# Performance work log

Hardware: AMD Instinct MI355X
Metric: run time of the kernel (lower is better)

Reference implementation:

```python
import jax, jax.numpy as jnp
import numpy as np

EPS = 1e-8
D = 1024      # embedding_dim
NH = 4        # num_heads
HD = D // NH  # head_dim
B, S = 4, 2048


def setup_inputs() -> dict:
    key = jax.random.key(0)
    k1, k2 = jax.random.split(key)
    x = jax.random.normal(k1, (B, S, 4 * D), dtype=jnp.float32)
    # small-init std = sqrt(2/(5*head_dim)) as in reset_parameters
    std = float(np.sqrt(2.0 / (5.0 * HD)))
    gate_weights = jax.random.normal(k2, (4, NH, HD, HD), dtype=jnp.float32) * std
    # biases: z,i,o zero; f gets powerlaw init (block 0 of 1 -> exponent 0.3)
    term = jnp.arange(HD, dtype=jnp.float32) / (HD - 1.0)
    f_bias = -(-5.0 + 12.0 * term ** 0.3)  # [HD]
    gate_biases = jnp.zeros((4, NH, HD), dtype=jnp.float32)
    gate_biases = gate_biases.at[2].set(jnp.broadcast_to(f_bias, (NH, HD)))
    return {"x_gate_inputs": x, "gate_weights": gate_weights, "gate_biases": gate_biases}


def _slstm_forward(x, W, biases):
    Bn, Sn, _ = x.shape
    # split into 4 gate pre-activations and apply headwise linear per gate
    xg = x.reshape(Bn, Sn, 4, NH, HD)           # gate order z,i,f,o along axis 2
    xg = jnp.moveaxis(xg, 2, 0)                  # [4,B,S,NH,HD]
    # headwise projection: einsum over head-in dim, per gate g and head h
    gates = jnp.einsum('gbshi,ghoi->gbsho', xg, W) + biases[:, None, None]  # [4,B,S,NH,HD]
    gates = jnp.moveaxis(gates, 2, 0)            # [S,4,B,NH,HD] for scan over time

    h0 = jnp.zeros((Bn, NH, HD), dtype=x.dtype)
    carry0 = (h0, h0, h0, jnp.zeros((Bn, NH, HD), dtype=jnp.float32))

    def step(carry, g_t):
        h, c, n, m = carry
        z_b, i_b, f_b, o_b = g_t[0], g_t[1], g_t[2], g_t[3]
        z_val = jnp.tanh(z_b)
        o_val = jax.nn.sigmoid(o_b)
        # faithful to original: exp then log(.+EPS), in m-state dtype (fp32)
        log_f = jnp.log(jnp.exp(f_b).astype(jnp.float32) + EPS)
        log_i = jnp.log(jnp.exp(i_b).astype(jnp.float32) + EPS)
        m_new = jnp.maximum(log_f + m, log_i)
        i_hat = jnp.exp(log_i - m_new).astype(x.dtype)
        f_hat = jnp.exp(log_f + m - m_new).astype(x.dtype)
        c_new = f_hat * c + i_hat * z_val
        n_new = f_hat * n + i_hat
        h_new = o_val * (c_new / (n_new + EPS))
        return (h_new, c_new, n_new, m_new), h_new

    (h_f, c_f, n_f, m_f), hs = jax.lax.scan(step, carry0, gates)
    h_seq = jnp.moveaxis(hs, 0, 1)               # [B,S,NH,HD]
    return h_seq, (h_f, c_f, n_f, m_f)


def reference(x_gate_inputs, gate_weights, gate_biases):
    h_seq, (h_f, c_f, n_f, m_f) = _slstm_forward(x_gate_inputs, gate_weights, gate_biases)
    return h_seq, h_f, c_f, n_f, m_f
```

## Files before the change

### kernel.cpp

```cpp
#include <hip/hip_runtime.h>
#include <cstdint>

#define S_LEN   2048
#define BATCH   4
#define NCH     4096
#define PLANE   ((size_t)S_LEN * NCH)
#define CHUNK   32
#define NCHUNK  64
#define SN      ((size_t)NCHUNK * NCH)
#define EPS     1e-8f

using bf16x8 = __attribute__((ext_vector_type(8))) short;
using f32x4  = __attribute__((ext_vector_type(4))) float;
typedef unsigned short u16;

__device__ __forceinline__ short f2bf(float f) {
  uint32_t u = __builtin_bit_cast(uint32_t, f);
  u += 0x7fffu + ((u >> 16) & 1u);
  return (short)(u >> 16);
}
__device__ __forceinline__ float bf2f(u16 u) {
  return __builtin_bit_cast(float, (uint32_t)u << 16);
}

__global__ __launch_bounds__(1024) void gates_gemm3(
    const float* __restrict__ x, const float* __restrict__ W,
    const float* __restrict__ bias,
    u16* __restrict__ gz16, float* __restrict__ gi, float* __restrict__ gf,
    u16* __restrict__ go16) {
  __shared__ u16 As[2][16 * 264];

  const int gh  = blockIdx.x;
  const int rg  = blockIdx.y;
  const int g   = gh >> 2, hh = gh & 3;
  const int tid = threadIdx.x;
  const int wave = tid >> 6, lane = tid & 63;
  const int l16 = lane & 15, quad = lane >> 4;
  const int n0  = wave * 16;
  const int row0 = rg * 256;

  bf16x8 Bf[8];
  {
    const float* wp = W + ((size_t)gh << 16) + (n0 + l16) * 256 + quad * 8;
#pragma unroll
    for (int kt = 0; kt < 8; ++kt) {
      float4 w0 = *(const float4*)(wp + kt * 32);
      float4 w1 = *(const float4*)(wp + kt * 32 + 4);
      bf16x8 b;
      b[0] = f2bf(w0.x); b[1] = f2bf(w0.y); b[2] = f2bf(w0.z); b[3] = f2bf(w0.w);
      b[4] = f2bf(w1.x); b[5] = f2bf(w1.y); b[6] = f2bf(w1.z); b[7] = f2bf(w1.w);
      Bf[kt] = b;
    }
  }
  const float bv = bias[gh * 256 + n0 + l16];

  const int sr = tid >> 6, sc = tid & 63;
  const float* sbase = x + (size_t)(row0 + sr) * 4096 + g * 1024 + hh * 256 + sc * 4;

  float4 sreg;
  auto gload = [&](int t) { sreg = *(const float4*)(sbase + (size_t)t * 16 * 4096); };
  auto swrite = [&](int buf) {
    ushort4 u;
    u.x = (u16)f2bf(sreg.x); u.y = (u16)f2bf(sreg.y);
    u.z = (u16)f2bf(sreg.z); u.w = (u16)f2bf(sreg.w);
    *(ushort4*)&As[buf][sr * 264 + sc * 4] = u;
  };

  gload(0); swrite(0);
  __syncthreads();

  for (int t = 0; t < 16; ++t) {
    if (t + 1 < 16) gload(t + 1);

    f32x4 acc = (f32x4){0.f, 0.f, 0.f, 0.f};
#pragma unroll
    for (int kt = 0; kt < 8; ++kt) {
      bf16x8 a = *(const bf16x8*)&As[t & 1][l16 * 264 + kt * 32 + quad * 8];
      acc = __builtin_amdgcn_mfma_f32_16x16x32_bf16(a, Bf[kt], acc, 0, 0, 0);
    }

#pragma unroll
    for (int rr = 0; rr < 4; ++rr) {
      int rowi = row0 + t * 16 + quad * 4 + rr;
      int sx = rowi & (S_LEN - 1);
      int bx = rowi >> 11;
      size_t idx = (size_t)sx * NCH + bx * 1024 + hh * 256 + n0 + l16;
      float v = acc[rr] + bv;
      if (g == 1)      gi[idx] = v;
      else if (g == 2) gf[idx] = v;
      else if (g == 0) {
        float tz = 1.f - 2.f * __builtin_amdgcn_rcpf(1.f + __expf(2.f * v));
        gz16[idx] = (u16)f2bf(tz);
      } else {
        float s = __builtin_amdgcn_rcpf(1.f + __expf(-v));
        go16[idx] = (u16)f2bf(s);
      }
    }

    if (t + 1 < 16) {
      swrite((t + 1) & 1);
      __syncthreads();
    }
  }
}

__global__ __launch_bounds__(256) void scan_pass1(
    const u16* __restrict__ gz16, const float* __restrict__ gi,
    const float* __restrict__ gf, float* __restrict__ sums) {
  const int t  = blockIdx.x * 256 + threadIdx.x;
  const int ch = t & (NCH - 1);
  const int ck = t >> 12;
  const size_t base = (size_t)ck * CHUNK * NCH + ch;

  float A = 0.f, Bv = -1e30f, D = 0.f, Dn = 0.f;

  float z0[8], i0[8], f0[8], z1[8], i1[8], f1[8];
#pragma unroll
  for (int j = 0; j < 8; ++j) {
    size_t off = base + (size_t)j * NCH;
    z0[j] = bf2f(gz16[off]); i0[j] = gi[off]; f0[j] = gf[off];
  }

  auto step = [&](float z, float i, float f) {
    float Bn = fmaxf(Bv + f, i);
    float e1 = __expf(Bv + f - Bn);
    float e2 = __expf(i - Bn);
    D  = e1 * D + e2 * z;
    Dn = e1 * Dn + e2;
    A += f;
    Bv = Bn;
  };

  for (int gb = 0; gb < 4; gb += 2) {
#pragma unroll
    for (int j = 0; j < 8; ++j) {
      size_t off = base + (size_t)((gb + 1) * 8 + j) * NCH;
      z1[j] = bf2f(gz16[off]); i1[j] = gi[off]; f1[j] = gf[off];
    }
#pragma unroll
    for (int j = 0; j < 8; ++j) step(z0[j], i0[j], f0[j]);
    if (gb + 2 < 4) {
#pragma unroll
      for (int j = 0; j < 8; ++j) {
        size_t off = base + (size_t)((gb + 2) * 8 + j) * NCH;
        z0[j] = bf2f(gz16[off]); i0[j] = gi[off]; f0[j] = gf[off];
      }
    }
#pragma unroll
    for (int j = 0; j < 8; ++j) step(z1[j], i1[j], f1[j]);
  }

  const size_t idx = (size_t)ck * NCH + ch;
  sums[idx]          = A;
  sums[SN + idx]     = Bv;
  sums[2 * SN + idx] = D;
  sums[3 * SN + idx] = Dn;
}

__global__ __launch_bounds__(256) void scan_pass2(
    const float* __restrict__ sums, float* __restrict__ ent) {
  const int ch = blockIdx.x * 256 + threadIdx.x;
  float c = 0.f, n = 0.f, m = 0.f;

  float A0 = sums[ch], B0 = sums[SN + ch], D0 = sums[2 * SN + ch], N0 = sums[3 * SN + ch];
  for (int k = 0; k < NCHUNK; ++k) {
    float A1 = 0.f, B1 = 0.f, D1 = 0.f, N1 = 0.f;
    if (k + 1 < NCHUNK) {
      size_t ni = (size_t)(k + 1) * NCH + ch;
      A1 = sums[ni]; B1 = sums[SN + ni]; D1 = sums[2 * SN + ni]; N1 = sums[3 * SN + ni];
    }
    size_t idx = (size_t)k * NCH + ch;
    ent[idx]          = c;
    ent[SN + idx]     = n;
    ent[2 * SN + idx] = m;
    float mo = fmaxf(m + A0, B0);
    float ea = __expf(m + A0 - mo);
    float eb = __expf(B0 - mo);
    c = ea * c + eb * D0;
    n = ea * n + eb * N0;
    m = mo;
    A0 = A1; B0 = B1; D0 = D1; N0 = N1;
  }
}

__global__ __launch_bounds__(256) void scan_pass3(
    const u16* __restrict__ gz16, const float* __restrict__ gi,
    const float* __restrict__ gf, const u16* __restrict__ go16,
    const float* __restrict__ ent, float* __restrict__ out) {
  const int t  = blockIdx.x * 256 + threadIdx.x;
  const int ch = t & (NCH - 1);
  const int ck = t >> 12;

  const size_t idx0 = (size_t)ck * NCH + ch;
  float c = ent[idx0];
  float n = ent[SN + idx0];
  float m = ent[2 * SN + idx0];

  const int b = ch >> 10, d = ch & 1023;
  const size_t base = (size_t)ck * CHUNK * NCH + ch;
  float* hout = out + (size_t)b * (S_LEN * 1024) + (size_t)(ck * CHUNK) * 1024 + d;

  float hv = 0.f;
  float z0[8], i0[8], f0[8], o0[8], z1[8], i1[8], f1[8], o1[8];
#pragma unroll
  for (int j = 0; j < 8; ++j) {
    size_t off = base + (size_t)j * NCH;
    z0[j] = bf2f(gz16[off]); i0[j] = gi[off]; f0[j] = gf[off]; o0[j] = bf2f(go16[off]);
  }

  auto step = [&](float z, float i, float f, float o, int s) {
    float mn = fmaxf(f + m, i);
    float fh = __expf(f + m - mn);
    float ih = __expf(i - mn);
    c = fh * c + ih * z;
    n = fh * n + ih;
    m = mn;
    hv = o * c * __builtin_amdgcn_rcpf(n + EPS);
    hout[(size_t)s * 1024] = hv;
  };

  for (int gb = 0; gb < 4; gb += 2) {
#pragma unroll
    for (int j = 0; j < 8; ++j) {
      size_t off = base + (size_t)((gb + 1) * 8 + j) * NCH;
      z1[j] = bf2f(gz16[off]); i1[j] = gi[off]; f1[j] = gf[off]; o1[j] = bf2f(go16[off]);
    }
#pragma unroll
    for (int j = 0; j < 8; ++j) step(z0[j], i0[j], f0[j], o0[j], gb * 8 + j);
    if (gb + 2 < 4) {
#pragma unroll
      for (int j = 0; j < 8; ++j) {
        size_t off = base + (size_t)((gb + 2) * 8 + j) * NCH;
        z0[j] = bf2f(gz16[off]); i0[j] = gi[off]; f0[j] = gf[off]; o0[j] = bf2f(go16[off]);
      }
    }
#pragma unroll
    for (int j = 0; j < 8; ++j) step(z1[j], i1[j], f1[j], o1[j], (gb + 1) * 8 + j);
  }

  if (ck == NCHUNK - 1) {
    float* fin = out + (size_t)BATCH * S_LEN * 1024;
    fin[ch]            = hv;
    fin[NCH + ch]      = c;
    fin[2 * NCH + ch]  = n;
    fin[3 * NCH + ch]  = m;
  }
}

extern "C" void kernel_launch(void* const* d_in, const int* in_sizes, int n_in,
                              void* d_out, int out_size, void* d_ws, size_t ws_size,
                              hipStream_t stream) {
  const float* x    = (const float*)d_in[0];
  const float* W    = (const float*)d_in[1];
  const float* bias = (const float*)d_in[2];
  float* out = (float*)d_out;

  u16*   gz16 = (u16*)d_ws;
  float* gi   = (float*)(gz16 + PLANE);
  float* gf   = gi + PLANE;
  u16*   go16 = (u16*)(gf + PLANE);
  float* sums = (float*)(go16 + PLANE);
  float* ent  = sums + 4 * SN;

  gates_gemm3<<<dim3(16, 32), dim3(1024), 0, stream>>>(x, W, bias, gz16, gi, gf, go16);
  scan_pass1<<<dim3(1024), dim3(256), 0, stream>>>(gz16, gi, gf, sums);
  scan_pass2<<<dim3(16), dim3(256), 0, stream>>>(sums, ent);
  scan_pass3<<<dim3(1024), dim3(256), 0, stream>>>(gz16, gi, gf, go16, ent, out);
}
```

Measured before the change: 277.8 us.

## Parallelize chunk-carry scan across wave lanes and double GEMM row tile

The pass-2 chunk combine changes from a per-channel sequential loop over 64 chunks into a warp-level Hillis-Steele prefix scan using shuffles, one lane per chunk. This removes a long serial dependency chain that ran on only 16 blocks. The gate GEMM also processes 32 rows per iteration with two MFMA accumulators, a padded LDS stride and deeper register prefetch, so fewer barriers are needed. The cost is more shuffle/exp work per channel and higher register use in the GEMM.

After: 308.3 us. +11.0%, slower.

```diff
diff --git a/kernel.cpp b/kernel.cpp
--- a/kernel.cpp
+++ b/kernel.cpp
@@ -9,6 +9,7 @@
 #define NCHUNK  64
 #define SN      ((size_t)NCHUNK * NCH)
 #define EPS     1e-8f
+#define LDST    280
 
 using bf16x8 = __attribute__((ext_vector_type(8))) short;
 using f32x4  = __attribute__((ext_vector_type(4))) float;
@@ -23,12 +24,12 @@
   return __builtin_bit_cast(float, (uint32_t)u << 16);
 }
 
-__global__ __launch_bounds__(1024) void gates_gemm3(
+__global__ __launch_bounds__(1024) void gates_gemm4(
     const float* __restrict__ x, const float* __restrict__ W,
     const float* __restrict__ bias,
     u16* __restrict__ gz16, float* __restrict__ gi, float* __restrict__ gf,
     u16* __restrict__ go16) {
-  __shared__ u16 As[2][16 * 264];
+  __shared__ u16 As[2][32 * LDST];
 
   const int gh  = blockIdx.x;
   const int rg  = blockIdx.y;
@@ -57,50 +58,63 @@
   const int sr = tid >> 6, sc = tid & 63;
   const float* sbase = x + (size_t)(row0 + sr) * 4096 + g * 1024 + hh * 256 + sc * 4;
 
-  float4 sreg;
-  auto gload = [&](int t) { sreg = *(const float4*)(sbase + (size_t)t * 16 * 4096); };
-  auto swrite = [&](int buf) {
-    ushort4 u;
-    u.x = (u16)f2bf(sreg.x); u.y = (u16)f2bf(sreg.y);
-    u.z = (u16)f2bf(sreg.z); u.w = (u16)f2bf(sreg.w);
-    *(ushort4*)&As[buf][sr * 264 + sc * 4] = u;
+  float4 pre[2][2];
+  auto gload = [&](int slot, int t) {
+    const float* p = sbase + (size_t)t * 32 * 4096;
+    pre[slot][0] = *(const float4*)p;
+    pre[slot][1] = *(const float4*)(p + 16 * 4096);
   };
-
-  gload(0); swrite(0);
+  auto swrite = [&](int slot, int buf) {
+#pragma unroll
+    for (int rh = 0; rh < 2; ++rh) {
+      float4 v = pre[slot][rh];
+      ushort4 u;
+      u.x = (u16)f2bf(v.x); u.y = (u16)f2bf(v.y);
+      u.z = (u16)f2bf(v.z); u.w = (u16)f2bf(v.w);
+      *(ushort4*)&As[buf][(sr + rh * 16) * LDST + sc * 4] = u;
+    }
+  };
+
+  gload(0, 0);
+  gload(1, 1);
+  swrite(0, 0);
   __syncthreads();
 
-  for (int t = 0; t < 16; ++t) {
-    if (t + 1 < 16) gload(t + 1);
-
-    f32x4 acc = (f32x4){0.f, 0.f, 0.f, 0.f};
+  for (int t = 0; t < 8; ++t) {
+    if (t + 2 < 8) gload(t & 1, t + 2);
+    if (t + 1 < 8) swrite((t + 1) & 1, (t + 1) & 1);
+
+    f32x4 acc0 = (f32x4){0.f, 0.f, 0.f, 0.f};
+    f32x4 acc1 = (f32x4){0.f, 0.f, 0.f, 0.f};
 #pragma unroll
     for (int kt = 0; kt < 8; ++kt) {
-      bf16x8 a = *(const bf16x8*)&As[t & 1][l16 * 264 + kt * 32 + quad * 8];
-      acc = __builtin_amdgcn_mfma_f32_16x16x32_bf16(a, Bf[kt], acc, 0, 0, 0);
-    }
-
-#pragma unroll
-    for (int rr = 0; rr < 4; ++rr) {
-      int rowi = row0 + t * 16 + quad * 4 + rr;
-      int sx = rowi & (S_LEN - 1);
-      int bx = rowi >> 11;
-      size_t idx = (size_t)sx * NCH + bx * 1024 + hh * 256 + n0 + l16;
-      float v = acc[rr] + bv;
-      if (g == 1)      gi[idx] = v;
-      else if (g == 2) gf[idx] = v;
-      else if (g == 0) {
-        float tz = 1.f - 2.f * __builtin_amdgcn_rcpf(1.f + __expf(2.f * v));
-        gz16[idx] = (u16)f2bf(tz);
-      } else {
-        float s = __builtin_amdgcn_rcpf(1.f + __expf(-v));
-        go16[idx] = (u16)f2bf(s);
+      bf16x8 a0 = *(const bf16x8*)&As[t & 1][l16 * LDST + kt * 32 + quad * 8];
+      bf16x8 a1 = *(const bf16x8*)&As[t & 1][(l16 + 16) * LDST + kt * 32 + quad * 8];
+      acc0 = __builtin_amdgcn_mfma_f32_16x16x32_bf16(a0, Bf[kt], acc0, 0, 0, 0);
+      acc1 = __builtin_amdgcn_mfma_f32_16x16x32_bf16(a1, Bf[kt], acc1, 0, 0, 0);
+    }
+
+#pragma unroll
+    for (int rt = 0; rt < 2; ++rt) {
+#pragma unroll
+      for (int rr = 0; rr < 4; ++rr) {
+        int rowi = row0 + t * 32 + rt * 16 + quad * 4 + rr;
+        int sx = rowi & (S_LEN - 1);
+        int bx = rowi >> 11;
+        size_t idx = (size_t)sx * NCH + bx * 1024 + hh * 256 + n0 + l16;
+        float v = (rt ? acc1[rr] : acc0[rr]) + bv;
+        if (g == 1)      gi[idx] = v;
+        else if (g == 2) gf[idx] = v;
+        else if (g == 0) {
+          float tz = 1.f - 2.f * __builtin_amdgcn_rcpf(1.f + __expf(2.f * v));
+          gz16[idx] = (u16)f2bf(tz);
+        } else {
+          float s = __builtin_amdgcn_rcpf(1.f + __expf(-v));
+          go16[idx] = (u16)f2bf(s);
+        }
       }
     }
-
-    if (t + 1 < 16) {
-      swrite((t + 1) & 1);
-      __syncthreads();
-    }
+    __syncthreads();
   }
 }
 
@@ -159,28 +173,51 @@
 
 __global__ __launch_bounds__(256) void scan_pass2(
     const float* __restrict__ sums, float* __restrict__ ent) {
-  const int ch = blockIdx.x * 256 + threadIdx.x;
-  float c = 0.f, n = 0.f, m = 0.f;
-
-  float A0 = sums[ch], B0 = sums[SN + ch], D0 = sums[2 * SN + ch], N0 = sums[3 * SN + ch];
-  for (int k = 0; k < NCHUNK; ++k) {
-    float A1 = 0.f, B1 = 0.f, D1 = 0.f, N1 = 0.f;
-    if (k + 1 < NCHUNK) {
-      size_t ni = (size_t)(k + 1) * NCH + ch;
-      A1 = sums[ni]; B1 = sums[SN + ni]; D1 = sums[2 * SN + ni]; N1 = sums[3 * SN + ni];
-    }
-    size_t idx = (size_t)k * NCH + ch;
-    ent[idx]          = c;
-    ent[SN + idx]     = n;
-    ent[2 * SN + idx] = m;
-    float mo = fmaxf(m + A0, B0);
-    float ea = __expf(m + A0 - mo);
-    float eb = __expf(B0 - mo);
-    c = ea * c + eb * D0;
-    n = ea * n + eb * N0;
-    m = mo;
-    A0 = A1; B0 = B1; D0 = D1; N0 = N1;
-  }
+  const int gt   = blockIdx.x * 256 + threadIdx.x;
+  const int ch   = gt >> 6;
+  const int lane = gt & 63;
+
+  const size_t idx = (size_t)lane * NCH + ch;
+  float A = sums[idx];
+  float B = sums[SN + idx];
+  float D = sums[2 * SN + idx];
+  float N = sums[3 * SN + idx];
+
+#pragma unroll
+  for (int d = 1; d < 64; d <<= 1) {
+    float A1 = __shfl_up(A, d, 64);
+    float B1 = __shfl_up(B, d, 64);
+    float D1 = __shfl_up(D, d, 64);
+    float N1 = __shfl_up(N, d, 64);
+    if (lane >= d) {
+      float Bn = fmaxf(B1 + A, B);
+      float e1 = __expf(B1 + A - Bn);
+      float e2 = __expf(B - Bn);
+      D = e1 * D1 + e2 * D;
+      N = e1 * N1 + e2 * N;
+      A = A + A1;
+      B = Bn;
+    }
+  }
+
+  float Ae = __shfl_up(A, 1, 64);
+  float Be = __shfl_up(B, 1, 64);
+  float De = __shfl_up(D, 1, 64);
+  float Ne = __shfl_up(N, 1, 64);
+
+  float c, n, m;
+  if (lane == 0) {
+    c = 0.f; n = 0.f; m = 0.f;
+  } else {
+    m = fmaxf(Ae, Be);
+    float eb = __expf(Be - m);
+    c = eb * De;
+    n = eb * Ne;
+  }
+
+  ent[idx]          = c;
+  ent[SN + idx]     = n;
+  ent[2 * SN + idx] = m;
 }
 
 __global__ __launch_bounds__(256) void scan_pass3(
@@ -262,8 +299,8 @@
   float* sums = (float*)(go16 + PLANE);
   float* ent  = sums + 4 * SN;
 
-  gates_gemm3<<<dim3(16, 32), dim3(1024), 0, stream>>>(x, W, bias, gz16, gi, gf, go16);
+  gates_gemm4<<<dim3(16, 32), dim3(1024), 0, stream>>>(x, W, bias, gz16, gi, gf, go16);
   scan_pass1<<<dim3(1024), dim3(256), 0, stream>>>(gz16, gi, gf, sums);
-  scan_pass2<<<dim3(16), dim3(256), 0, stream>>>(sums, ent);
+  scan_pass2<<<dim3(1024), dim3(256), 0, stream>>>(sums, ent);
   scan_pass3<<<dim3(1024), dim3(256), 0, stream>>>(gz16, gi, gf, go16, ent, out);
 }
```

## Store i/f gates as fp16, halve scan chunk, parallelize chunk-carry scan via shuffles

Applied to the files above, without the earlier changes.

Stores the i and f gate pre-activations as fp16 instead of fp32, cutting intermediate write and read traffic. Halves the chunk length to 16 so that passes 1 and 3 launch twice as many threads and each thread loads all of its data up front. Replaces the serial 64-step carry propagation in pass 2 with a wave-wide Hillis-Steele scan over 128 chunks using shuffles, launched on many more blocks. This risks precision loss from fp16 storage of log-domain gates, and doubles the size of the chunk summary buffers.

Measured after the change: 278.4 us. No clear change (+0.2%).

```diff
diff --git a/kernel.cpp b/kernel.cpp
--- a/kernel.cpp
+++ b/kernel.cpp
@@ -5,8 +5,8 @@
 #define BATCH   4
 #define NCH     4096
 #define PLANE   ((size_t)S_LEN * NCH)
-#define CHUNK   32
-#define NCHUNK  64
+#define CHUNK   16
+#define NCHUNK  128
 #define SN      ((size_t)NCHUNK * NCH)
 #define EPS     1e-8f
 
@@ -22,11 +22,18 @@
 __device__ __forceinline__ float bf2f(u16 u) {
   return __builtin_bit_cast(float, (uint32_t)u << 16);
 }
-
-__global__ __launch_bounds__(1024) void gates_gemm3(
+__device__ __forceinline__ u16 f2h(float f) {
+  _Float16 h = (_Float16)f;
+  return __builtin_bit_cast(unsigned short, h);
+}
+__device__ __forceinline__ float h2f(u16 u) {
+  return (float)__builtin_bit_cast(_Float16, u);
+}
+
+__global__ __launch_bounds__(1024) void gates_gemm6(
     const float* __restrict__ x, const float* __restrict__ W,
     const float* __restrict__ bias,
-    u16* __restrict__ gz16, float* __restrict__ gi, float* __restrict__ gf,
+    u16* __restrict__ gz16, u16* __restrict__ gi16, u16* __restrict__ gf16,
     u16* __restrict__ go16) {
   __shared__ u16 As[2][16 * 264];
 
@@ -86,8 +93,8 @@
       int bx = rowi >> 11;
       size_t idx = (size_t)sx * NCH + bx * 1024 + hh * 256 + n0 + l16;
       float v = acc[rr] + bv;
-      if (g == 1)      gi[idx] = v;
-      else if (g == 2) gf[idx] = v;
+      if (g == 1)      gi16[idx] = f2h(v);
+      else if (g == 2) gf16[idx] = f2h(v);
       else if (g == 0) {
         float tz = 1.f - 2.f * __builtin_amdgcn_rcpf(1.f + __expf(2.f * v));
         gz16[idx] = (u16)f2bf(tz);
@@ -105,8 +112,8 @@
 }
 
 __global__ __launch_bounds__(256) void scan_pass1(
-    const u16* __restrict__ gz16, const float* __restrict__ gi,
-    const float* __restrict__ gf, float* __restrict__ sums) {
+    const u16* __restrict__ gz16, const u16* __restrict__ gi16,
+    const u16* __restrict__ gf16, float* __restrict__ sums) {
   const int t  = blockIdx.x * 256 + threadIdx.x;
   const int ch = t & (NCH - 1);
   const int ck = t >> 12;
@@ -118,7 +125,12 @@
 #pragma unroll
   for (int j = 0; j < 8; ++j) {
     size_t off = base + (size_t)j * NCH;
-    z0[j] = bf2f(gz16[off]); i0[j] = gi[off]; f0[j] = gf[off];
+    z0[j] = bf2f(gz16[off]); i0[j] = h2f(gi16[off]); f0[j] = h2f(gf16[off]);
+  }
+#pragma unroll
+  for (int j = 0; j < 8; ++j) {
+    size_t off = base + (size_t)(8 + j) * NCH;
+    z1[j] = bf2f(gz16[off]); i1[j] = h2f(gi16[off]); f1[j] = h2f(gf16[off]);
   }
 
   auto step = [&](float z, float i, float f) {
@@ -131,24 +143,10 @@
     Bv = Bn;
   };
 
-  for (int gb = 0; gb < 4; gb += 2) {
-#pragma unroll
-    for (int j = 0; j < 8; ++j) {
-      size_t off = base + (size_t)((gb + 1) * 8 + j) * NCH;
-      z1[j] = bf2f(gz16[off]); i1[j] = gi[off]; f1[j] = gf[off];
-    }
-#pragma unroll
-    for (int j = 0; j < 8; ++j) step(z0[j], i0[j], f0[j]);
-    if (gb + 2 < 4) {
-#pragma unroll
-      for (int j = 0; j < 8; ++j) {
-        size_t off = base + (size_t)((gb + 2) * 8 + j) * NCH;
-        z0[j] = bf2f(gz16[off]); i0[j] = gi[off]; f0[j] = gf[off];
-      }
-    }
-#pragma unroll
-    for (int j = 0; j < 8; ++j) step(z1[j], i1[j], f1[j]);
-  }
+#pragma unroll
+  for (int j = 0; j < 8; ++j) step(z0[j], i0[j], f0[j]);
+#pragma unroll
+  for (int j = 0; j < 8; ++j) step(z1[j], i1[j], f1[j]);
 
   const size_t idx = (size_t)ck * NCH + ch;
   sums[idx]          = A;
@@ -159,33 +157,72 @@
 
 __global__ __launch_bounds__(256) void scan_pass2(
     const float* __restrict__ sums, float* __restrict__ ent) {
-  const int ch = blockIdx.x * 256 + threadIdx.x;
-  float c = 0.f, n = 0.f, m = 0.f;
-
-  float A0 = sums[ch], B0 = sums[SN + ch], D0 = sums[2 * SN + ch], N0 = sums[3 * SN + ch];
-  for (int k = 0; k < NCHUNK; ++k) {
-    float A1 = 0.f, B1 = 0.f, D1 = 0.f, N1 = 0.f;
-    if (k + 1 < NCHUNK) {
-      size_t ni = (size_t)(k + 1) * NCH + ch;
-      A1 = sums[ni]; B1 = sums[SN + ni]; D1 = sums[2 * SN + ni]; N1 = sums[3 * SN + ni];
-    }
-    size_t idx = (size_t)k * NCH + ch;
-    ent[idx]          = c;
-    ent[SN + idx]     = n;
-    ent[2 * SN + idx] = m;
-    float mo = fmaxf(m + A0, B0);
-    float ea = __expf(m + A0 - mo);
-    float eb = __expf(B0 - mo);
-    c = ea * c + eb * D0;
-    n = ea * n + eb * N0;
-    m = mo;
-    A0 = A1; B0 = B1; D0 = D1; N0 = N1;
+  const int gt   = blockIdx.x * 256 + threadIdx.x;
+  const int ch   = gt >> 6;
+  const int lane = gt & 63;
+
+  const size_t i0 = (size_t)(2 * lane) * NCH + ch;
+  const size_t i1 = (size_t)(2 * lane + 1) * NCH + ch;
+  float A0 = sums[i0], B0 = sums[SN + i0], D0 = sums[2 * SN + i0], N0 = sums[3 * SN + i0];
+  float A1 = sums[i1], B1 = sums[SN + i1], D1 = sums[2 * SN + i1], N1 = sums[3 * SN + i1];
+
+  float A, B, D, N;
+  {
+    float Bn = fmaxf(B0 + A1, B1);
+    D = __expf(B0 + A1 - Bn) * D0 + __expf(B1 - Bn) * D1;
+    N = __expf(B0 + A1 - Bn) * N0 + __expf(B1 - Bn) * N1;
+    A = A0 + A1;
+    B = Bn;
+  }
+
+#pragma unroll
+  for (int d = 1; d < 64; d <<= 1) {
+    float Ae = __shfl_up(A, d, 64);
+    float Be = __shfl_up(B, d, 64);
+    float De = __shfl_up(D, d, 64);
+    float Ne = __shfl_up(N, d, 64);
+    if (lane >= d) {
+      float Bn = fmaxf(Be + A, B);
+      float e1 = __expf(Be + A - Bn);
+      float e2 = __expf(B - Bn);
+      D = e1 * De + e2 * D;
+      N = e1 * Ne + e2 * N;
+      A = A + Ae;
+      B = Bn;
+    }
+  }
+
+  float Ae = __shfl_up(A, 1, 64);
+  float Be = __shfl_up(B, 1, 64);
+  float De = __shfl_up(D, 1, 64);
+  float Ne = __shfl_up(N, 1, 64);
+  if (lane == 0) { Ae = 0.f; Be = -1e30f; De = 0.f; Ne = 0.f; }
+
+  {
+    float m = fmaxf(Ae, Be);
+    float eb = __expf(Be - m);
+    ent[i0]          = eb * De;
+    ent[SN + i0]     = eb * Ne;
+    ent[2 * SN + i0] = m;
+  }
+  {
+    float Bf_ = fmaxf(Be + A0, B0);
+    float e1 = __expf(Be + A0 - Bf_);
+    float e2 = __expf(B0 - Bf_);
+    float Df_ = e1 * De + e2 * D0;
+    float Nf_ = e1 * Ne + e2 * N0;
+    float Af_ = Ae + A0;
+    float m = fmaxf(Af_, Bf_);
+    float eb = __expf(Bf_ - m);
+    ent[i1]          = eb * Df_;
+    ent[SN + i1]     = eb * Nf_;
+    ent[2 * SN + i1] = m;
   }
 }
 
 __global__ __launch_bounds__(256) void scan_pass3(
-    const u16* __restrict__ gz16, const float* __restrict__ gi,
-    const float* __restrict__ gf, const u16* __restrict__ go16,
+    const u16* __restrict__ gz16, const u16* __restrict__ gi16,
+    const u16* __restrict__ gf16, const u16* __restrict__ go16,
     const float* __restrict__ ent, float* __restrict__ out) {
   const int t  = blockIdx.x * 256 + threadIdx.x;
   const int ch = t & (NCH - 1);
@@ -205,7 +242,14 @@
 #pragma unroll
   for (int j = 0; j < 8; ++j) {
     size_t off = base + (size_t)j * NCH;
-    z0[j] = bf2f(gz16[off]); i0[j] = gi[off]; f0[j] = gf[off]; o0[j] = bf2f(go16[off]);
+    z0[j] = bf2f(gz16[off]); i0[j] = h2f(gi16[off]);
+    f0[j] = h2f(gf16[off]); o0[j] = bf2f(go16[off]);
+  }
+#pragma unroll
+  for (int j = 0; j < 8; ++j) {
+    size_t off = base + (size_t)(8 + j) * NCH;
+    z1[j] = bf2f(gz16[off]); i1[j] = h2f(gi16[off]);
+    f1[j] = h2f(gf16[off]); o1[j] = bf2f(go16[off]);
   }
 
   auto step = [&](float z, float i, float f, float o, int s) {
@@ -219,24 +263,10 @@
     hout[(size_t)s * 1024] = hv;
   };
 
-  for (int gb = 0; gb < 4; gb += 2) {
-#pragma unroll
-    for (int j = 0; j < 8; ++j) {
-      size_t off = base + (size_t)((gb + 1) * 8 + j) * NCH;
-      z1[j] = bf2f(gz16[off]); i1[j] = gi[off]; f1[j] = gf[off]; o1[j] = bf2f(go16[off]);
-    }
-#pragma unroll
-    for (int j = 0; j < 8; ++j) step(z0[j], i0[j], f0[j], o0[j], gb * 8 + j);
-    if (gb + 2 < 4) {
-#pragma unroll
-      for (int j = 0; j < 8; ++j) {
-        size_t off = base + (size_t)((gb + 2) * 8 + j) * NCH;
-        z0[j] = bf2f(gz16[off]); i0[j] = gi[off]; f0[j] = gf[off]; o0[j] = bf2f(go16[off]);
-      }
-    }
-#pragma unroll
-    for (int j = 0; j < 8; ++j) step(z1[j], i1[j], f1[j], o1[j], (gb + 1) * 8 + j);
-  }
+#pragma unroll
+  for (int j = 0; j < 8; ++j) step(z0[j], i0[j], f0[j], o0[j], j);
+#pragma unroll
+  for (int j = 0; j < 8; ++j) step(z1[j], i1[j], f1[j], o1[j], 8 + j);
 
   if (ck == NCHUNK - 1) {
     float* fin = out + (size_t)BATCH * S_LEN * 1024;
@@ -256,14 +286,14 @@
   float* out = (float*)d_out;
 
   u16*   gz16 = (u16*)d_ws;
-  float* gi   = (float*)(gz16 + PLANE);
-  float* gf   = gi + PLANE;
-  u16*   go16 = (u16*)(gf + PLANE);
+  u16*   gi16 = gz16 + PLANE;
+  u16*   gf16 = gi16 + PLANE;
+  u16*   go16 = gf16 + PLANE;
   float* sums = (float*)(go16 + PLANE);
   float* ent  = sums + 4 * SN;
 
-  gates_gemm3<<<dim3(16, 32), dim3(1024), 0, stream>>>(x, W, bias, gz16, gi, gf, go16);
-  scan_pass1<<<dim3(1024), dim3(256), 0, stream>>>(gz16, gi, gf, sums);
-  scan_pass2<<<dim3(16), dim3(256), 0, stream>>>(sums, ent);
-  scan_pass3<<<dim3(1024), dim3(256), 0, stream>>>(gz16, gi, gf, go16, ent, out);
-}
+  gates_gemm6<<<dim3(16, 32), dim3(1024), 0, stream>>>(x, W, bias, gz16, gi16, gf16, go16);
+  scan_pass1<<<dim3(2048), dim3(256), 0, stream>>>(gz16, gi16, gf16, sums);
+  scan_pass2<<<dim3(1024), dim3(256), 0, stream>>>(sums, ent);
+  scan_pass3<<<dim3(2048), dim3(256), 0, stream>>>(gz16, gi16, gf16, go16, ent, out);
+}
```
